# Kernel tuning notes

Hardware: AMD Instinct MI355X
Metric: run time of the kernel (lower is better)

## Reference

```python
import jax, jax.numpy as jnp
import numpy as np
import math

B, T, D = 4, 2048, 1024
H = 16            # n_heads
HD = D // H       # head_dim = 64
LAT = 128         # latent_dim
ROPE = 32         # rope_dim
EPS = 1e-6


def rms_norm(x, g):
    rms = jnp.sqrt(jnp.mean(x * x, axis=-1, keepdims=True) + EPS)
    return g * (x / rms)


def setup_inputs() -> dict:
    key = jax.random.key(0)
    ks = jax.random.split(key, 7)
    s = lambda fan_in: 1.0 / math.sqrt(fan_in)
    x = jax.random.normal(ks[0], (B, T, D), dtype=jnp.float32)
    Wq = jax.random.normal(ks[1], (D, D), dtype=jnp.float32) * s(D)
    Wkv = jax.random.normal(ks[2], (D, LAT), dtype=jnp.float32) * s(D)
    Wk = jax.random.normal(ks[3], (LAT, H * ROPE), dtype=jnp.float32) * s(LAT)
    Wv = jax.random.normal(ks[4], (LAT, H * (HD - ROPE)), dtype=jnp.float32) * s(LAT)
    Wo = jax.random.normal(ks[5], (D, D), dtype=jnp.float32) * s(D)
    q_g = jnp.ones((HD,), dtype=jnp.float32)
    k_g = jnp.ones((ROPE,), dtype=jnp.float32)
    return {"x": x, "Wq": Wq, "Wkv": Wkv, "Wk": Wk, "Wv": Wv, "Wo": Wo,
            "q_g": q_g, "k_g": k_g}


def reference(x, Wq, Wkv, Wk, Wv, Wo, q_g, k_g):
    b, t, d = x.shape
    # Q projection -> (b, h, t, hd), RMSNorm over head_dim
    q = (x @ Wq).reshape(b, t, H, HD).transpose(0, 2, 1, 3)
    q = rms_norm(q, q_g)
    # KV latent compression
    kv = x @ Wkv                                   # (b, t, LAT)
    k = (kv @ Wk).reshape(b, t, H, ROPE).transpose(0, 2, 1, 3)   # (b,h,t,rope)
    k = rms_norm(k, k_g)
    v_c = (kv @ Wv).reshape(b, t, H, HD - ROPE).transpose(0, 2, 1, 3)
    # K is zero-padded to head_dim, so only the first ROPE dims of q contribute
    scores = jnp.einsum('bhtr,bhsr->bhts', q[..., :ROPE], k) / math.sqrt(HD)
    causal = jnp.triu(jnp.ones((t, t), dtype=bool), k=1)
    scores = jnp.where(causal, -jnp.inf, scores)
    probs = jax.nn.softmax(scores, axis=-1)        # (b, h, t, s)
    # V is zero-padded at the end by ROPE dims -> compute then pad
    out_c = jnp.einsum('bhts,bhsd->bhtd', probs, v_c)   # (b,h,t,HD-ROPE)
    out = jnp.pad(out_c, ((0, 0), (0, 0), (0, 0), (0, ROPE)))
    out = out.transpose(0, 2, 1, 3).reshape(b, t, d)
    return out @ Wo
```

## Files before the change

kernel.cpp:

```cpp
#include <hip/hip_runtime.h>
#include <hip/hip_bf16.h>
#include <math.h>

using bf16 = __hip_bfloat16;
typedef __attribute__((ext_vector_type(8))) short bf16x8;
typedef __attribute__((ext_vector_type(4))) float f32x4;

#define BB   4
#define TT   2048
#define DD   1024
#define HH   16
#define HD_  64
#define LAT_ 128
#define RP   32
#define EPS_ 1e-6f

static __device__ __forceinline__ void stf(float* p, float v) { *p = v; }
static __device__ __forceinline__ void stf(bf16* p, float v) { *p = __float2bfloat16(v); }

static __device__ __forceinline__ void gl2lds16(const void* g, void* l)
{
    __builtin_amdgcn_global_load_lds(
        (const __attribute__((address_space(1))) void*)g,
        (__attribute__((address_space(3))) void*)l, 16, 0, 0);
}

__global__ __launch_bounds__(256)
void sentinel_kernel(float* __restrict__ out, float val, long long n)
{
    long long i = (long long)blockIdx.x * 256 + threadIdx.x;
    if (i < n) out[i] = val;
}

__global__ __launch_bounds__(256)
void conv_x_kernel(const float* __restrict__ x, bf16* __restrict__ xb, long long n4)
{
    long long i = (long long)blockIdx.x * 256 + threadIdx.x;
    if (i >= n4) return;
    float4 v = *(const float4*)(x + i * 4);
    union { bf16 h[4]; uint2 u; } o;
    o.h[0] = __float2bfloat16(v.x);
    o.h[1] = __float2bfloat16(v.y);
    o.h[2] = __float2bfloat16(v.z);
    o.h[3] = __float2bfloat16(v.w);
    *(uint2*)(xb + i * 4) = o.u;
}

__global__ __launch_bounds__(256)
void conv_trans_kernel(const float* __restrict__ W, bf16* __restrict__ WT,
                       int K, int N)
{
    __shared__ __align__(16) bf16 t[64][72];
    const int k0 = blockIdx.y * 64, n0 = blockIdx.x * 64;
    const int tid = threadIdx.x;
    const int r = tid >> 2, c0 = (tid & 3) * 16;
    const float* src = W + (size_t)(k0 + r) * N + n0 + c0;
    #pragma unroll
    for (int j = 0; j < 16; j += 4) {
        float4 v = *(const float4*)(src + j);
        t[c0 + j + 0][r] = __float2bfloat16(v.x);
        t[c0 + j + 1][r] = __float2bfloat16(v.y);
        t[c0 + j + 2][r] = __float2bfloat16(v.z);
        t[c0 + j + 3][r] = __float2bfloat16(v.w);
    }
    __syncthreads();
    const int rr = tid >> 2, cc = (tid & 3) * 16;
    bf16* dst = WT + (size_t)(n0 + rr) * K + k0 + cc;
    *(bf16x8*)dst       = *(const bf16x8*)&t[rr][cc];
    *(bf16x8*)(dst + 8) = *(const bf16x8*)&t[rr][cc + 8];
}

__global__ __launch_bounds__(256)
void conv_wkwv_kernel(const float* __restrict__ Wk, const float* __restrict__ Wv,
                      bf16* __restrict__ WT)
{
    int idx = blockIdx.x * 256 + threadIdx.x;
    if (idx >= 128 * 1024) return;
    int k = idx >> 10, n = idx & 1023;
    float v = (n < 512) ? Wk[k * 512 + n] : Wv[k * 512 + (n - 512)];
    WT[(size_t)n * 128 + k] = __float2bfloat16(v);
}

__global__ __launch_bounds__(256)
void conv_woT_kernel(const float* __restrict__ Wo, bf16* __restrict__ WT)
{
    __shared__ __align__(16) bf16 t[64][72];
    const int mm0 = blockIdx.y * 64, n0 = blockIdx.x * 64;
    const int tid = threadIdx.x;
    const int r = tid >> 2, c0 = (tid & 3) * 16;
    const int mm = mm0 + r;
    const int row = ((mm >> 5) << 6) | (mm & 31);
    const float* src = Wo + (size_t)row * 1024 + n0 + c0;
    #pragma unroll
    for (int j = 0; j < 16; j += 4) {
        float4 v = *(const float4*)(src + j);
        t[c0 + j + 0][r] = __float2bfloat16(v.x);
        t[c0 + j + 1][r] = __float2bfloat16(v.y);
        t[c0 + j + 2][r] = __float2bfloat16(v.z);
        t[c0 + j + 3][r] = __float2bfloat16(v.w);
    }
    __syncthreads();
    const int rr = tid >> 2, cc = (tid & 3) * 16;
    bf16* dst = WT + (size_t)(n0 + rr) * 512 + mm0 + cc;
    *(bf16x8*)dst       = *(const bf16x8*)&t[rr][cc];
    *(bf16x8*)(dst + 8) = *(const bf16x8*)&t[rr][cc + 8];
}

#define GEMM_PROLOG_128 \
    __shared__ __align__(16) short As[128][32]; \
    __shared__ __align__(16) short Bs[128][32]; \
    const int tid  = threadIdx.x; \
    const int wave = tid >> 6, lane = tid & 63; \
    const int quad = lane >> 4, l16 = lane & 15; \
    const int wr = (wave >> 1) * 64, wc = (wave & 1) * 64; \
    const int row0 = blockIdx.y * 128, col0 = blockIdx.x * 128; \
    const int srow = tid >> 2, scol = (tid & 3) * 8; \
    char* lAs0 = (char*)As + wave * 1024; \
    char* lAs1 = (char*)As + 4096 + wave * 1024; \
    char* lBs0 = (char*)Bs + wave * 1024; \
    char* lBs1 = (char*)Bs + 4096 + wave * 1024; \
    f32x4 acc[4][4]; \
    _Pragma("unroll") \
    for (int mt = 0; mt < 4; ++mt) \
        _Pragma("unroll") \
        for (int nt = 0; nt < 4; ++nt) \
            acc[mt][nt] = (f32x4){0.f, 0.f, 0.f, 0.f}; \
    for (int k0 = 0; k0 < K; k0 += 32) { \
        const short* ga = A  + (size_t)(row0 + srow) * K + k0 + scol; \
        const short* gb = BT + (size_t)(col0 + srow) * K + k0 + scol; \
        __syncthreads(); \
        gl2lds16(ga,                  lAs0); \
        gl2lds16(ga + (size_t)64 * K, lAs1); \
        gl2lds16(gb,                  lBs0); \
        gl2lds16(gb + (size_t)64 * K, lBs1); \
        __syncthreads(); \
        bf16x8 af[4], bfv[4]; \
        _Pragma("unroll") \
        for (int mt = 0; mt < 4; ++mt) \
            af[mt] = *(const bf16x8*)&As[wr + mt * 16 + l16][quad * 8]; \
        _Pragma("unroll") \
        for (int nt = 0; nt < 4; ++nt) \
            bfv[nt] = *(const bf16x8*)&Bs[wc + nt * 16 + l16][quad * 8]; \
        _Pragma("unroll") \
        for (int mt = 0; mt < 4; ++mt) \
            _Pragma("unroll") \
            for (int nt = 0; nt < 4; ++nt) \
                acc[mt][nt] = __builtin_amdgcn_mfma_f32_16x16x32_bf16( \
                    af[mt], bfv[nt], acc[mt][nt], 0, 0, 0); \
    }

template <typename OT>
__global__ __launch_bounds__(256)
void gemm_mfma(const short* __restrict__ A, const short* __restrict__ BT,
               OT* __restrict__ C, int M, int N, int K)
{
    GEMM_PROLOG_128
    #pragma unroll
    for (int mt = 0; mt < 4; ++mt)
        #pragma unroll
        for (int nt = 0; nt < 4; ++nt) {
            const int col = col0 + wc + nt * 16 + l16;
            #pragma unroll
            for (int r = 0; r < 4; ++r) {
                const int row = row0 + wr + mt * 16 + quad * 4 + r;
                stf(C + (size_t)row * N + col, acc[mt][nt][r]);
            }
        }
}

__global__ __launch_bounds__(256)
void gemm_qrms(const short* __restrict__ A, const short* __restrict__ BT,
               bf16* __restrict__ qn, const float* __restrict__ qg,
               int M, int N, int K)
{
    GEMM_PROLOG_128
    const int h = (col0 + wc) >> 6;
    const float g0 = qg[l16], g1 = qg[16 + l16];
    #pragma unroll
    for (int mt = 0; mt < 4; ++mt) {
        float ss[4];
        #pragma unroll
        for (int r = 0; r < 4; ++r)
            ss[r] = acc[mt][0][r] * acc[mt][0][r] + acc[mt][1][r] * acc[mt][1][r]
                  + acc[mt][2][r] * acc[mt][2][r] + acc[mt][3][r] * acc[mt][3][r];
        #pragma unroll
        for (int off = 1; off < 16; off <<= 1)
            #pragma unroll
            for (int r = 0; r < 4; ++r) ss[r] += __shfl_xor(ss[r], off, 64);
        #pragma unroll
        for (int r = 0; r < 4; ++r) {
            const float inv = 0.125f / sqrtf(ss[r] * (1.0f / HD_) + EPS_);
            const int row = row0 + wr + mt * 16 + quad * 4 + r;
            const int b = row >> 11, t = row & 2047;
            bf16* op = qn + (((size_t)(b * HH + h)) * TT + t) * RP;
            op[l16]      = __float2bfloat16(g0 * acc[mt][0][r] * inv);
            op[16 + l16] = __float2bfloat16(g1 * acc[mt][1][r] * inv);
        }
    }
}

__global__ __launch_bounds__(256)
void gemm_kv(const short* __restrict__ A, const short* __restrict__ BT,
             bf16* __restrict__ kn, bf16* __restrict__ vb,
             const float* __restrict__ kg, int M, int N, int K)
{
    GEMM_PROLOG_128
    const int colbase = col0 + wc;
    if (colbase < 512) {
        const int h0 = colbase >> 5;
        const float g0 = kg[l16], g1 = kg[16 + l16];
        #pragma unroll
        for (int mt = 0; mt < 4; ++mt) {
            float s0[4], s1[4];
            #pragma unroll
            for (int r = 0; r < 4; ++r) {
                s0[r] = acc[mt][0][r] * acc[mt][0][r] + acc[mt][1][r] * acc[mt][1][r];
                s1[r] = acc[mt][2][r] * acc[mt][2][r] + acc[mt][3][r] * acc[mt][3][r];
            }
            #pragma unroll
            for (int off = 1; off < 16; off <<= 1)
                #pragma unroll
                for (int r = 0; r < 4; ++r) {
                    s0[r] += __shfl_xor(s0[r], off, 64);
                    s1[r] += __shfl_xor(s1[r], off, 64);
                }
            #pragma unroll
            for (int r = 0; r < 4; ++r) {
                const float i0 = 1.0f / sqrtf(s0[r] * (1.0f / RP) + EPS_);
                const float i1 = 1.0f / sqrtf(s1[r] * (1.0f / RP) + EPS_);
                const int row = row0 + wr + mt * 16 + quad * 4 + r;
                const int b = row >> 11, t = row & 2047;
                bf16* op0 = kn + (((size_t)(b * HH + h0)) * TT + t) * RP;
                bf16* op1 = kn + (((size_t)(b * HH + h0 + 1)) * TT + t) * RP;
                op0[l16]      = __float2bfloat16(g0 * acc[mt][0][r] * i0);
                op0[16 + l16] = __float2bfloat16(g1 * acc[mt][1][r] * i0);
                op1[l16]      = __float2bfloat16(g0 * acc[mt][2][r] * i1);
                op1[16 + l16] = __float2bfloat16(g1 * acc[mt][3][r] * i1);
            }
        }
    } else {
        const int h0 = (colbase - 512) >> 5;
        #pragma unroll
        for (int mt = 0; mt < 4; ++mt)
            #pragma unroll
            for (int r = 0; r < 4; ++r) {
                const int row = row0 + wr + mt * 16 + quad * 4 + r;
                const int b = row >> 11, t = row & 2047;
                bf16* op0 = vb + (((size_t)(b * HH + h0)) * TT + t) * RP;
                bf16* op1 = vb + (((size_t)(b * HH + h0 + 1)) * TT + t) * RP;
                op0[l16]      = __float2bfloat16(acc[mt][0][r]);
                op0[16 + l16] = __float2bfloat16(acc[mt][1][r]);
                op1[l16]      = __float2bfloat16(acc[mt][2][r]);
                op1[16 + l16] = __float2bfloat16(acc[mt][3][r]);
            }
    }
}

__global__ __launch_bounds__(256)
void gemm_k64(const short* __restrict__ A, const short* __restrict__ BT,
              bf16* __restrict__ C, int M, int N, int K)
{
    __shared__ __align__(16) short As[64][32];
    __shared__ __align__(16) short Bs[128][32];
    const int tid  = threadIdx.x;
    const int wave = tid >> 6, lane = tid & 63;
    const int quad = lane >> 4, l16 = lane & 15;
    const int wr = (wave >> 1) * 32, wc = (wave & 1) * 64;
    const int row0 = blockIdx.y * 64, col0 = blockIdx.x * 128;
    const int srow = tid >> 2, scol = (tid & 3) * 8;

    char* lAs  = (char*)As + wave * 1024;
    char* lBs0 = (char*)Bs + wave * 1024;
    char* lBs1 = (char*)Bs + 4096 + wave * 1024;

    f32x4 acc[2][4];
    #pragma unroll
    for (int mt = 0; mt < 2; ++mt)
        #pragma unroll
        for (int nt = 0; nt < 4; ++nt)
            acc[mt][nt] = (f32x4){0.f, 0.f, 0.f, 0.f};

    for (int k0 = 0; k0 < K; k0 += 32) {
        const short* ga = A  + (size_t)(row0 + srow) * K + k0 + scol;
        const short* gb = BT + (size_t)(col0 + srow) * K + k0 + scol;
        __syncthreads();
        gl2lds16(ga,                  lAs);
        gl2lds16(gb,                  lBs0);
        gl2lds16(gb + (size_t)64 * K, lBs1);
        __syncthreads();

        bf16x8 af[2], bfv[4];
        #pragma unroll
        for (int mt = 0; mt < 2; ++mt)
            af[mt] = *(const bf16x8*)&As[wr + mt * 16 + l16][quad * 8];
        #pragma unroll
        for (int nt = 0; nt < 4; ++nt)
            bfv[nt] = *(const bf16x8*)&Bs[wc + nt * 16 + l16][quad * 8];
        #pragma unroll
        for (int mt = 0; mt < 2; ++mt)
            #pragma unroll
            for (int nt = 0; nt < 4; ++nt)
                acc[mt][nt] = __builtin_amdgcn_mfma_f32_16x16x32_bf16(
                    af[mt], bfv[nt], acc[mt][nt], 0, 0, 0);
    }

    #pragma unroll
    for (int mt = 0; mt < 2; ++mt)
        #pragma unroll
        for (int nt = 0; nt < 4; ++nt) {
            const int col = col0 + wc + nt * 16 + l16;
            #pragma unroll
            for (int r = 0; r < 4; ++r) {
                const int row = row0 + wr + mt * 16 + quad * 4 + r;
                C[(size_t)row * N + col] = __float2bfloat16(acc[mt][nt][r]);
            }
        }
}

__global__ __launch_bounds__(256)
void vtrans_kernel(const bf16* __restrict__ vb, bf16* __restrict__ vT)
{
    __shared__ __align__(16) short tile[32][72];
    const int bh = blockIdx.y;
    const int t0 = blockIdx.x * 64;
    const int tid = threadIdx.x;
    const int tl = tid >> 2, c0 = (tid & 3) * 8;
    bf16x8 v = *(const bf16x8*)(vb + ((size_t)bh * TT + t0 + tl) * RP + c0);
    #pragma unroll
    for (int j = 0; j < 8; ++j) tile[c0 + j][tl] = v[j];
    __syncthreads();
    const int c = tid >> 3, tt = (tid & 7) * 8;
    bf16x8 o = *(const bf16x8*)&tile[c][tt];
    *(bf16x8*)(vT + ((size_t)bh * RP + c) * TT + t0 + tt) = o;
}

struct __attribute__((aligned(8))) bf4 { bf16 v[4]; };

__global__ __launch_bounds__(512, 4)
void attn_mfma(const bf16* __restrict__ qn, const bf16* __restrict__ kn,
               const bf16* __restrict__ vT, bf16* __restrict__ att)
{
    __shared__ __align__(16) short KsF[64 * 32];
    __shared__ __align__(16) short VsF[32 * 64];
    __shared__ __align__(16) bf16 P_lds[8][16][72];
    const int tid  = threadIdx.x;
    const int w8   = tid >> 6, lane = tid & 63;
    const int quad = lane >> 4, l16 = lane & 15;
    const int f  = (int)(blockIdx.y * 8 + blockIdx.x);
    const int xr = f & 7, j = f >> 3;
    const int bx = j & 7;
    const int bh = xr + 8 * (j >> 3);
    const int b = bh >> 4, h = bh & 15;

    const bf16* knb = kn + (size_t)bh * TT * RP;
    const bf16* vtb = vT + (size_t)bh * RP * TT;

    const bool isK = (w8 < 4);
    const int  cK = tid;
    const int  cV = tid - 256;
    const bf16* sBase = isK
        ? knb + (size_t)(cK >> 2) * RP + ((cK & 3) ^ ((cK >> 3) & 3)) * 8
        : vtb + (size_t)(cV >> 3) * TT + ((cV & 7) ^ ((cV >> 3) & 7)) * 8;
    const int  sMult = isK ? RP : 1;
    char* ldsDst = isK ? ((char*)KsF + w8 * 1024)
                       : ((char*)VsF + (w8 - 4) * 1024);

    const int kslot = ((l16 >> 1) & 3);
    const int vswz = (l16 & 7);

    #pragma unroll 1
    for (int pi = 0; pi < 2; ++pi) {
        const int qt = pi ? (15 - bx) : bx;
        const int NT = 2 * qt + 2;
        const int qbase = qt * 128 + w8 * 16;

        bf16x8 qf = *(const bf16x8*)(qn + ((size_t)bh * TT + qbase + l16) * RP + quad * 8);

        float lsum = 0.f;
        f32x4 oacc0 = (f32x4){0.f, 0.f, 0.f, 0.f};
        f32x4 oacc1 = (f32x4){0.f, 0.f, 0.f, 0.f};

        for (int st = 0; st < NT; ++st) {
            const int s0 = st * 64;
            __syncthreads();
            gl2lds16(sBase + (size_t)s0 * sMult, ldsDst);
            __syncthreads();

            f32x4 sc[4];
            #pragma unroll
            for (int sub = 0; sub < 4; ++sub) {
                bf16x8 kf = *(const bf16x8*)&KsF[(sub * 16 + l16) * 32
                                                 + ((quad ^ kslot) * 8)];
                sc[sub] = __builtin_amdgcn_mfma_f32_16x16x32_bf16(
                    kf, qf, (f32x4){0.f, 0.f, 0.f, 0.f}, 0, 0, 0);
            }

            if (s0 + 63 > qbase) {
                const int qg_ = qbase + l16;
                #pragma unroll
                for (int sub = 0; sub < 4; ++sub)
                    #pragma unroll
                    for (int r = 0; r < 4; ++r)
                        if (s0 + sub * 16 + quad * 4 + r > qg_) sc[sub][r] = -1e30f;
            }

            #pragma unroll
            for (int sub = 0; sub < 4; ++sub) {
                const float p0 = __expf(sc[sub][0]);
                const float p1 = __expf(sc[sub][1]);
                const float p2 = __expf(sc[sub][2]);
                const float p3 = __expf(sc[sub][3]);
                bf4 pk;
                pk.v[0] = __float2bfloat16(p0);
                pk.v[1] = __float2bfloat16(p1);
                pk.v[2] = __float2bfloat16(p2);
                pk.v[3] = __float2bfloat16(p3);
                *(bf4*)&P_lds[w8][l16][sub * 16 + quad * 4] = pk;
                lsum += (p0 + p1) + (p2 + p3);
            }

            #pragma unroll
            for (int ks = 0; ks < 2; ++ks) {
                bf16x8 pf  = *(const bf16x8*)&P_lds[w8][l16][ks * 32 + quad * 8];
                bf16x8 vf0 = *(const bf16x8*)&VsF[l16 * 64
                                + (((ks * 4 + quad) ^ vswz) * 8)];
                bf16x8 vf1 = *(const bf16x8*)&VsF[(16 + l16) * 64
                                + (((ks * 4 + quad) ^ vswz) * 8)];
                oacc0 = __builtin_amdgcn_mfma_f32_16x16x32_bf16(pf, vf0, oacc0, 0, 0, 0);
                oacc1 = __builtin_amdgcn_mfma_f32_16x16x32_bf16(pf, vf1, oacc1, 0, 0, 0);
            }
        }

        lsum += __shfl_xor(lsum, 16, 64);
        lsum += __shfl_xor(lsum, 32, 64);
        #pragma unroll
        for (int r = 0; r < 4; ++r) {
            const float ls = __shfl(lsum, quad * 20 + r, 64);
            const float inv = 1.0f / ls;
            const int t = qbase + quad * 4 + r;
            bf16* op = att + ((size_t)(b * TT + t)) * 512 + h * 32;
            op[l16]      = __float2bfloat16(oacc0[r] * inv);
            op[16 + l16] = __float2bfloat16(oacc1[r] * inv);
        }
    }
}

extern "C" void kernel_launch(void* const* d_in, const int* in_sizes, int n_in,
                              void* d_out, int out_size, void* d_ws, size_t ws_size,
                              hipStream_t stream)
{
    float* out = (float*)d_out;
    const long long NOUT = (long long)BB * TT * DD;
    const int outgrid = (int)((NOUT + 255) / 256);

    static const long long expect[8] =
        {8388608, 1048576, 131072, 65536, 65536, 1048576, 64, 32};
    if (n_in != 8) {
        sentinel_kernel<<<outgrid, 256, 0, stream>>>(out, 20000.0f + 100.0f * n_in, NOUT);
        return;
    }
    for (int i = 0; i < 8; ++i) {
        if ((long long)in_sizes[i] != expect[i]) {
            sentinel_kernel<<<outgrid, 256, 0, stream>>>(out, 10000.0f + 1000.0f * i, NOUT);
            return;
        }
    }
    if (ws_size < 62914624ULL) {
        sentinel_kernel<<<outgrid, 256, 0, stream>>>(
            out, 30000.0f + (float)(ws_size >> 20), NOUT);
        return;
    }
    if (out_size != 8388608) {
        sentinel_kernel<<<outgrid, 256, 0, stream>>>(
            out, 512.0f * (1.0f + (float)(out_size >> 20)), NOUT);
        return;
    }

    const float* x   = (const float*)d_in[0];
    const float* Wq  = (const float*)d_in[1];
    const float* Wkv = (const float*)d_in[2];
    const float* Wk  = (const float*)d_in[3];
    const float* Wv  = (const float*)d_in[4];
    const float* Wo  = (const float*)d_in[5];
    const float* qg  = (const float*)d_in[6];
    const float* kg  = (const float*)d_in[7];

    char* base = (char*)d_ws + 64;
    bf16*  xb    = (bf16*)(base + 0);
    bf16*  wqT   = (bf16*)(base + 16777216);
    bf16*  wkvT  = (bf16*)(base + 18874368);
    bf16*  kvb   = (bf16*)(base + 19136512);
    bf16*  att_b = (bf16*)(base + 0);
    bf16*  vTb   = (bf16*)(base + 8388608);
    bf16*  qn    = (bf16*)(base + 35913728);
    bf16*  kn    = (bf16*)(base + 44302336);
    bf16*  vb    = (bf16*)(base + 52690944);
    bf16*  wkwvT = (bf16*)(base + 61079552);
    bf16*  woT   = (bf16*)(base + 61341696);

    const int BT = BB * TT;

    conv_x_kernel<<<outgrid / 4, 256, 0, stream>>>(x, xb, NOUT / 4);
    conv_trans_kernel<<<dim3(16, 16), 256, 0, stream>>>(Wq, wqT, 1024, 1024);
    conv_trans_kernel<<<dim3(2, 16), 256, 0, stream>>>(Wkv, wkvT, 1024, 128);
    conv_wkwv_kernel<<<512, 256, 0, stream>>>(Wk, Wv, wkwvT);
    conv_woT_kernel<<<dim3(16, 8), 256, 0, stream>>>(Wo, woT);

    gemm_qrms<<<dim3(8, 64), 256, 0, stream>>>(
        (const short*)xb, (const short*)wqT, qn, qg, BT, DD, DD);
    gemm_k64<<<dim3(1, 128), 256, 0, stream>>>(
        (const short*)xb, (const short*)wkvT, kvb, BT, LAT_, DD);
    gemm_kv<<<dim3(8, 64), 256, 0, stream>>>(
        (const short*)kvb, (const short*)wkwvT, kn, vb, kg, BT, 2 * 512, LAT_);
    vtrans_kernel<<<dim3(32, 64), 256, 0, stream>>>(vb, vTb);
    attn_mfma<<<dim3(8, 64), 512, 0, stream>>>(qn, kn, vTb, att_b);
    gemm_mfma<float><<<dim3(8, 64), 256, 0, stream>>>(
        (const short*)att_b, (const short*)woT, out, BT, DD, 512);
}
```

Baseline: 235.4 us.

## Double-buffer K/V LDS tiles in attention with next-tile prefetch

Splits the K and V shared-memory tiles into two buffers. The async global-to-LDS load for the next key tile is issued before computing on the current one, so load latency can overlap the MFMA and softmax work. Each iteration now has one explicit vmcnt wait plus barrier instead of two __syncthreads. The trade-off is extra LDS use and one prefetch past the last needed tile, which reads a little beyond the current head's data.

```diff
diff --git a/kernel.cpp b/kernel.cpp
--- a/kernel.cpp
+++ b/kernel.cpp
@@ -340,8 +340,8 @@
 void attn_mfma(const bf16* __restrict__ qn, const bf16* __restrict__ kn,
                const bf16* __restrict__ vT, bf16* __restrict__ att)
 {
-    __shared__ __align__(16) short KsF[64 * 32];
-    __shared__ __align__(16) short VsF[32 * 64];
+    __shared__ __align__(16) short KsF[2][64 * 32];
+    __shared__ __align__(16) short VsF[2][32 * 64];
     __shared__ __align__(16) bf16 P_lds[8][16][72];
     const int tid  = threadIdx.x;
     const int w8   = tid >> 6, lane = tid & 63;
@@ -361,12 +361,11 @@
     const bf16* sBase = isK
         ? knb + (size_t)(cK >> 2) * RP + ((cK & 3) ^ ((cK >> 3) & 3)) * 8
         : vtb + (size_t)(cV >> 3) * TT + ((cV & 7) ^ ((cV >> 3) & 7)) * 8;
-    const int  sMult = isK ? RP : 1;
-    char* ldsDst = isK ? ((char*)KsF + w8 * 1024)
-                       : ((char*)VsF + (w8 - 4) * 1024);
+    const long long sStep = (long long)(isK ? RP : 1) * 64;
+    const int ldsOff = isK ? w8 * 1024 : (w8 - 4) * 1024;
 
     const int kslot = ((l16 >> 1) & 3);
-    const int vswz = (l16 & 7);
+    const int vswz  = (l16 & 7);
 
     #pragma unroll 1
     for (int pi = 0; pi < 2; ++pi) {
@@ -374,22 +373,34 @@
         const int NT = 2 * qt + 2;
         const int qbase = qt * 128 + w8 * 16;
 
+        if (pi) {
+            asm volatile("s_waitcnt vmcnt(0)\n\ts_barrier" ::: "memory");
+        }
+
         bf16x8 qf = *(const bf16x8*)(qn + ((size_t)bh * TT + qbase + l16) * RP + quad * 8);
 
         float lsum = 0.f;
         f32x4 oacc0 = (f32x4){0.f, 0.f, 0.f, 0.f};
         f32x4 oacc1 = (f32x4){0.f, 0.f, 0.f, 0.f};
 
+        gl2lds16(sBase, (isK ? (char*)KsF[0] : (char*)VsF[0]) + ldsOff);
+        int cur = 0;
+
         for (int st = 0; st < NT; ++st) {
+            asm volatile("s_waitcnt vmcnt(0)\n\ts_barrier" ::: "memory");
+
+            const int nxt = cur ^ 1;
+            gl2lds16(sBase + (long long)(st + 1) * sStep,
+                     (isK ? (char*)KsF[nxt] : (char*)VsF[nxt]) + ldsOff);
+
             const int s0 = st * 64;
-            __syncthreads();
-            gl2lds16(sBase + (size_t)s0 * sMult, ldsDst);
-            __syncthreads();
+            const short* KsC = KsF[cur];
+            const short* VsC = VsF[cur];
 
             f32x4 sc[4];
             #pragma unroll
             for (int sub = 0; sub < 4; ++sub) {
-                bf16x8 kf = *(const bf16x8*)&KsF[(sub * 16 + l16) * 32
+                bf16x8 kf = *(const bf16x8*)&KsC[(sub * 16 + l16) * 32
                                                  + ((quad ^ kslot) * 8)];
                 sc[sub] = __builtin_amdgcn_mfma_f32_16x16x32_bf16(
                     kf, qf, (f32x4){0.f, 0.f, 0.f, 0.f}, 0, 0, 0);
@@ -422,13 +433,15 @@
             #pragma unroll
             for (int ks = 0; ks < 2; ++ks) {
                 bf16x8 pf  = *(const bf16x8*)&P_lds[w8][l16][ks * 32 + quad * 8];
-                bf16x8 vf0 = *(const bf16x8*)&VsF[l16 * 64
+                bf16x8 vf0 = *(const bf16x8*)&VsC[l16 * 64
                                 + (((ks * 4 + quad) ^ vswz) * 8)];
-                bf16x8 vf1 = *(const bf16x8*)&VsF[(16 + l16) * 64
+                bf16x8 vf1 = *(const bf16x8*)&VsC[(16 + l16) * 64
                                 + (((ks * 4 + quad) ^ vswz) * 8)];
                 oacc0 = __builtin_amdgcn_mfma_f32_16x16x32_bf16(pf, vf0, oacc0, 0, 0, 0);
                 oacc1 = __builtin_amdgcn_mfma_f32_16x16x32_bf16(pf, vf1, oacc1, 0, 0, 0);
             }
+
+            cur = nxt;
         }
 
         lsum += __shfl_xor(lsum, 16, 64);
```

After: 230.2 us. -2.2%, faster.
